# Kernel optimization log

Measured on AMD Instinct MI355X. Metric: run time of the kernel, lower is better.

The kernel has to match this reference:

```python
import jax, jax.numpy as jnp
import numpy as np

B, T, D = 2, 2048, 2048
H, HD = 8, 128
C = H * HD  # 1024 channels
BT = 64     # chunk size
EPS_RMS = 1.1920929e-07  # torch fp32 finfo eps (RMSNorm default)


def causal_dw_conv(x, w, b):
    # x: [B,T,C], w: [C,4], b: [C]. Equals torch Conv1d(groups=C, k=4, padding=3)[..., :T]
    Bx, Tx, Cx = x.shape
    xp = jnp.pad(x, ((0, 0), (3, 0), (0, 0)))
    out = sum(xp[:, j:j + Tx, :] * w[None, None, :, j] for j in range(4))
    return out + b


def chunk_kda(q, k, v, g):
    # q,k,g: [B,H,T,K]; v: [B,H,T,V]
    Bx, Hx, Tx, K = q.shape
    V = v.shape[-1]
    NT = Tx // BT
    resh = lambda a: a.reshape(Bx, Hx, NT, BT, a.shape[-1])
    q, k, v, g = map(resh, (q, k, v, g))
    gc = jnp.cumsum(g, axis=-2)                        # [B,H,NT,BT,K]
    diff = gc[..., :, None, :] - gc[..., None, :, :]   # [B,H,NT,BT,BT,K]
    tri_incl = jnp.tril(jnp.ones((BT, BT), bool))
    tri_strict = jnp.tril(jnp.ones((BT, BT), bool), -1)
    Aqk = jnp.einsum('bhnik,bhnjk,bhnijk->bhnij', q, k, jnp.exp(diff)) * tri_incl
    Akk = jnp.einsum('bhnik,bhnjk,bhnijk->bhnij', k, k, jnp.exp(-diff)) * tri_strict
    # UT transform: the in-place forward substitution in the source computes
    # A = (I + strictly_lower(Akk))^{-1}; apply it via a unit-lower triangular solve.
    M = Akk + jnp.eye(BT, dtype=q.dtype)
    rhs = jnp.concatenate([jnp.exp(gc) * k, v], axis=-1)
    sol = jax.scipy.linalg.solve_triangular(M, rhs, lower=True, unit_diagonal=True)
    w_, u = sol[..., :K], sol[..., K:]                 # w = A@(exp(gc)*k), u = A@v
    qg = q * jnp.exp(gc)

    def step(S, xs):
        qg_i, k_i, u_i, gc_i, w_i, Aqk_i = xs
        o_i = qg_i @ S + Aqk_i @ (u_i - w_i @ S)
        g_last = gc_i[:, :, -1]                        # [B,H,K]
        decay = jnp.exp(g_last[:, :, None, :] - gc_i)  # [B,H,BT,K]
        S = S * jnp.exp(g_last)[..., :, None] + jnp.einsum('bhck,bhcv->bhkv', k_i * decay, u_i)
        return S, o_i

    xs = tuple(jnp.moveaxis(a, 2, 0) for a in (qg, k, u, gc, w_, Aqk))
    S0 = jnp.zeros((Bx, Hx, K, V), q.dtype)
    S, o = jax.lax.scan(step, S0, xs)
    o = jnp.moveaxis(o, 0, 2).reshape(Bx, Hx, Tx, V)
    return o, S


def _forward(x, Wq, Wk, Wv, conv_q_w, conv_q_b, conv_k_w, conv_k_b, conv_v_w, conv_v_b,
             Wad, Wau, Wb, Wgd, Wgu, norm_w, Wo):
    Bx, Tx, Dx = x.shape
    heads = lambda y: y.reshape(Bx, Tx, H, HD).transpose(0, 2, 1, 3)
    q = heads(causal_dw_conv(x @ Wq, conv_q_w, conv_q_b))
    k = heads(causal_dw_conv(x @ Wk, conv_k_w, conv_k_b))
    q = q / jnp.maximum(jnp.linalg.norm(q, axis=-1, keepdims=True), 1e-12)
    k = k / jnp.maximum(jnp.linalg.norm(k, axis=-1, keepdims=True), 1e-12)
    v = heads(jax.nn.silu(causal_dw_conv(x @ Wv, conv_v_w, conv_v_b)))
    alpha = jax.nn.sigmoid(heads(x @ Wad @ Wau))
    g = jnp.log(jnp.clip(alpha, 1e-6, None))
    _beta = jax.nn.sigmoid(x @ Wb)  # computed in source but unused by chunk_kda
    o, S = chunk_kda(q, k, v, g)
    o = o.transpose(0, 2, 1, 3)                        # [B,T,H,HD]
    o = o * jax.lax.rsqrt(jnp.mean(o * o, axis=-1, keepdims=True) + EPS_RMS) * norm_w
    gate = jax.nn.sigmoid(x @ Wgd @ Wgu).reshape(Bx, Tx, H, HD)
    o = (o * gate).reshape(Bx, Tx, H * HD)
    return o @ Wo, S


def setup_inputs():
    key = jax.random.key(0)
    ks = jax.random.split(key, 16)
    n = lambda k, shape, s=0.02: jax.random.normal(k, shape, jnp.float32) * s
    return {
        'x': jax.random.normal(ks[0], (B, T, D), jnp.float32),
        'Wq': n(ks[1], (D, C)), 'Wk': n(ks[2], (D, C)), 'Wv': n(ks[3], (D, C)),
        'conv_q_w': n(ks[4], (C, 4), 0.1), 'conv_q_b': jnp.zeros((C,), jnp.float32),
        'conv_k_w': n(ks[5], (C, 4), 0.1), 'conv_k_b': jnp.zeros((C,), jnp.float32),
        'conv_v_w': n(ks[6], (C, 4), 0.1), 'conv_v_b': jnp.zeros((C,), jnp.float32),
        'Wad': n(ks[7], (D, HD)), 'Wau': n(ks[8], (HD, C)),
        'Wb': n(ks[9], (D, H)),
        'Wgd': n(ks[10], (D, HD)), 'Wgu': n(ks[11], (HD, C)),
        'norm_w': jnp.ones((HD,), jnp.float32),
        'Wo': n(ks[12], (C, D)),
    }


def reference(x, Wq, Wk, Wv, conv_q_w, conv_q_b, conv_k_w, conv_k_b, conv_v_w, conv_v_b,
              Wad, Wau, Wb, Wgd, Wgu, norm_w, Wo):
    return _forward(x, Wq, Wk, Wv, conv_q_w, conv_q_b, conv_k_w, conv_k_b, conv_v_w, conv_v_b,
                    Wad, Wau, Wb, Wgd, Wgu, norm_w, Wo)
```

## Files before the change

kernel.cpp:

```cpp
#include <hip/hip_runtime.h>
#include <hip/hip_bf16.h>
#include <cstdint>
#include <cstddef>

constexpr int B_  = 2;
constexpr int T_  = 2048;
constexpr int D_  = 2048;
constexpr int H_  = 8;
constexpr int HD_ = 128;
constexpr int C_  = 1024;
constexpr int BT_ = 64;
constexpr int NT_ = 32;
constexpr int M_  = 4096;
constexpr float EPS_RMS = 1.1920929e-07f;

typedef __bf16 bf16x8 __attribute__((ext_vector_type(8)));
typedef float f32x4 __attribute__((ext_vector_type(4)));

typedef const __attribute__((address_space(1))) unsigned int* gptr_t;
typedef __attribute__((address_space(3))) unsigned int* lptr_t;

__device__ __forceinline__ void gload16(const void* g, void* l) {
  __builtin_amdgcn_global_load_lds((gptr_t)g, (lptr_t)l, 16, 0, 0);
}


#define LD_A(base, mq, dst) do { \
    _Pragma("unroll") for (int i_ = 0; i_ < 4; ++i_) \
      _Pragma("unroll") for (int k_ = 0; k_ < 2; ++k_) \
        dst[i_][k_] = *(const bf16x8*)((base) + (mq) * 8192 + i_ * 2048 + k_ * 1024); \
  } while (0)

#define LD_B(base, nq, dst) do { \
    _Pragma("unroll") for (int j_ = 0; j_ < 2; ++j_) \
      _Pragma("unroll") for (int k_ = 0; k_ < 2; ++k_) \
        dst[j_][k_] = *(const bf16x8*)((base) + (nq) * 4096 + j_ * 2048 + k_ * 1024); \
  } while (0)

#define MM_Q(afr, bfr, mq, nq) do { \
    _Pragma("unroll") for (int i_ = 0; i_ < 4; ++i_) \
      _Pragma("unroll") for (int j_ = 0; j_ < 2; ++j_) \
        _Pragma("unroll") for (int k_ = 0; k_ < 2; ++k_) \
          acc[(mq) * 4 + i_][(nq) * 2 + j_] = __builtin_amdgcn_mfma_f32_16x16x32_bf16( \
              afr[i_][k_], bfr[j_][k_], acc[(mq) * 4 + i_][(nq) * 2 + j_], 0, 0, 0); \
  } while (0)

#define STAGE(src, grow0, kc, loff) do { \
    gload16((src) + (size_t)((grow0) + sr0) * 2048 + (kc) + sc0, smem + (loff) + tid * 16); \
    gload16((src) + (size_t)((grow0) + sr1) * 2048 + (kc) + sc1, smem + (loff) + 8192 + tid * 16); \
  } while (0)

#define PH_SYNC_PRE do { \
    __builtin_amdgcn_s_barrier(); \
    asm volatile("s_waitcnt lgkmcnt(0)" ::: "memory"); \
    __builtin_amdgcn_sched_barrier(0); \
    __builtin_amdgcn_s_setprio(1); \
  } while (0)

#define PH_SYNC_POST do { \
    __builtin_amdgcn_s_setprio(0); \
    __builtin_amdgcn_sched_barrier(0); \
    __builtin_amdgcn_s_barrier(); \
  } while (0)

#define PH_SYNC_POST_VM4 do { \
    __builtin_amdgcn_s_setprio(0); \
    __builtin_amdgcn_sched_barrier(0); \
    asm volatile("s_waitcnt vmcnt(4)" ::: "memory"); \
    __builtin_amdgcn_s_barrier(); \
  } while (0)

#define PH_SYNC_POST_VM0 do { \
    __builtin_amdgcn_s_setprio(0); \
    __builtin_amdgcn_sched_barrier(0); \
    asm volatile("s_waitcnt vmcnt(0)" ::: "memory"); \
    __builtin_amdgcn_s_barrier(); \
  } while (0)

__global__ __launch_bounds__(512, 1) void gemm8p(
    const __hip_bfloat16* __restrict__ A_, const __hip_bfloat16* __restrict__ B_,
    __hip_bfloat16* __restrict__ pre, __hip_bfloat16* __restrict__ adb,
    __hip_bfloat16* __restrict__ gdb) {
  __shared__ alignas(16) char smem[131072];
  const int tid = threadIdx.x, lane = tid & 63;
  const int wid = tid >> 6;
  const int wm = (wid >> 2) * 128, wn = (wid & 3) * 64;
  const int lr = lane & 15, lg = lane >> 4;

  const int bid = blockIdx.x;
  const int swz = (bid & 7) * 26 + (bid >> 3);
  const int mt = swz / 13, nt = swz % 13;
  const int m0 = mt * 256, n0g = nt * 256;

  int ob0 = tid * 16;         ob0 ^= ((ob0 >> 9) & 1) << 5;
  int ob1 = (tid + 512) * 16; ob1 ^= ((ob1 >> 9) & 1) << 5;
  const int sr0 = ((ob0 >> 11) << 4) + ((ob0 >> 6) & 15);
  const int sc0 = ((ob0 >> 10) & 1) * 32 + ((ob0 & 63) >> 1);
  const int sr1 = ((ob1 >> 11) << 4) + ((ob1 >> 6) & 15);
  const int sc1 = ((ob1 >> 10) & 1) * 32 + ((ob1 & 63) >> 1);

  const int foff = lr * 64 + ((lg * 16) ^ ((lr & 8) << 2));
  const int bq = (wn & 64) * 128;
  const char* a0base = smem + (wm >> 7) * 16384 + foff;
  const char* a1base = smem + 65536 + (wm >> 7) * 16384 + foff;
  const char* b0base = smem + 32768 + (wn >> 7) * 16384 + bq + foff;
  const char* b1base = smem + 98304 + (wn >> 7) * 16384 + bq + foff;

  f32x4 acc[8][4];
#pragma unroll
  for (int i = 0; i < 8; ++i)
#pragma unroll
    for (int j = 0; j < 4; ++j) acc[i][j] = (f32x4)(0.f);

  bf16x8 a[4][2], b01[2][2], b23[2][2];

  STAGE(A_, m0,        0, 0);
  STAGE(A_, m0 + 128,  0, 16384);
  STAGE(B_, n0g,       0, 32768);
  STAGE(B_, n0g + 128, 0, 32768 + 16384);
  STAGE(B_, n0g,       64, 98304);
  STAGE(B_, n0g + 128, 64, 98304 + 16384);
  asm volatile("s_waitcnt vmcnt(4)" ::: "memory");
  __builtin_amdgcn_s_barrier();

#pragma unroll 1
  for (int it = 0; it < 15; ++it) {
    const int kA1 = (2 * it + 1) * 64;
    const int kN2 = (2 * it + 2) * 64;
    const int kB3 = (2 * it + 3) * 64;
    LD_A(a0base, 0, a);
    LD_B(b0base, 0, b01);
    STAGE(A_, m0, kA1, 65536);
    PH_SYNC_PRE; MM_Q(a, b01, 0, 0); PH_SYNC_POST;
    LD_B(b0base, 1, b23);
    STAGE(A_, m0 + 128, kA1, 65536 + 16384);
    PH_SYNC_PRE; MM_Q(a, b23, 0, 1); PH_SYNC_POST;
    LD_A(a0base, 1, a);
    STAGE(B_, n0g, kN2, 32768);
    PH_SYNC_PRE; MM_Q(a, b23, 1, 1); PH_SYNC_POST;
    STAGE(B_, n0g + 128, kN2, 32768 + 16384);
    PH_SYNC_PRE; MM_Q(a, b01, 1, 0); PH_SYNC_POST_VM4;
    LD_A(a1base, 0, a);
    LD_B(b1base, 0, b01);
    STAGE(A_, m0, kN2, 0);
    PH_SYNC_PRE; MM_Q(a, b01, 0, 0); PH_SYNC_POST;
    LD_B(b1base, 1, b23);
    STAGE(A_, m0 + 128, kN2, 16384);
    PH_SYNC_PRE; MM_Q(a, b23, 0, 1); PH_SYNC_POST;
    LD_A(a1base, 1, a);
    STAGE(B_, n0g, kB3, 98304);
    PH_SYNC_PRE; MM_Q(a, b23, 1, 1); PH_SYNC_POST;
    STAGE(B_, n0g + 128, kB3, 98304 + 16384);
    PH_SYNC_PRE; MM_Q(a, b01, 1, 0); PH_SYNC_POST_VM4;
  }

  {
    const int kT = 1984;
    LD_A(a0base, 0, a);
    LD_B(b0base, 0, b01);
    STAGE(A_, m0, kT, 65536);
    PH_SYNC_PRE; MM_Q(a, b01, 0, 0); PH_SYNC_POST;
    LD_B(b0base, 1, b23);
    STAGE(A_, m0 + 128, kT, 65536 + 16384);
    PH_SYNC_PRE; MM_Q(a, b23, 0, 1); PH_SYNC_POST;
    LD_A(a0base, 1, a);
    PH_SYNC_PRE; MM_Q(a, b23, 1, 1); PH_SYNC_POST;
    PH_SYNC_PRE; MM_Q(a, b01, 1, 0); PH_SYNC_POST_VM0;
    LD_A(a1base, 0, a);
    LD_B(b1base, 0, b01);
    MM_Q(a, b01, 0, 0);
    LD_B(b1base, 1, b23);
    MM_Q(a, b23, 0, 1);
    LD_A(a1base, 1, a);
    MM_Q(a, b23, 1, 1);
    MM_Q(a, b01, 1, 0);
  }

#pragma unroll
  for (int mf = 0; mf < 8; ++mf) {
    const int row0 = m0 + wm + mf * 16 + lg * 4;
#pragma unroll
    for (int nf = 0; nf < 4; ++nf) {
      const int c = n0g + wn + nf * 16 + lr;
#pragma unroll
      for (int r = 0; r < 4; ++r) {
        const __hip_bfloat16 v = __float2bfloat16(acc[mf][nf][r]);
        const size_t rr = (size_t)(row0 + r);
        if (c < 3072)      pre[rr * 3072 + c] = v;
        else if (c < 3200) adb[rr * 128 + (c - 3072)] = v;
        else               gdb[rr * 128 + (c - 3200)] = v;
      }
    }
  }
}

template <typename OutT>
__global__ __launch_bounds__(256) void gemm_bf16k(
    const __hip_bfloat16* __restrict__ A, const __hip_bfloat16* __restrict__ Bt,
    OutT* __restrict__ C, int N, int K) {
  __shared__ __hip_bfloat16 sA[128 * 32];
  __shared__ __hip_bfloat16 sB[128 * 32];
  const int tid = threadIdx.x;
  const int lane = tid & 63;
  const int m0 = blockIdx.y * 128, n0 = blockIdx.x * 128;
  const int wm = ((tid >> 6) >> 1) * 64, wn = ((tid >> 6) & 1) * 64;
  f32x4 acc[4][4];
#pragma unroll
  for (int i = 0; i < 4; ++i)
#pragma unroll
    for (int j = 0; j < 4; ++j) acc[i][j] = (f32x4)(0.f);
  const int f0 = tid, f1 = tid + 256;
  const int r0 = f0 >> 2, c0 = (f0 & 3) * 8;
  const int r1 = f1 >> 2, c1 = (f1 & 3) * 8;
  const size_t aoff0 = (size_t)(m0 + r0) * K + c0;
  const size_t aoff1 = (size_t)(m0 + r1) * K + c1;
  const size_t boff0 = (size_t)(n0 + r0) * K + c0;
  const size_t boff1 = (size_t)(n0 + r1) * K + c1;
  const int lr = lane & 15, lk = (lane >> 4) * 8;
  for (int k0 = 0; k0 < K; k0 += 32) {
    __syncthreads();
    gload16(A + aoff0 + k0, &sA[f0 * 8]);
    gload16(A + aoff1 + k0, &sA[f1 * 8]);
    gload16(Bt + boff0 + k0, &sB[f0 * 8]);
    gload16(Bt + boff1 + k0, &sB[f1 * 8]);
    __syncthreads();
    bf16x8 af[4], bfr[4];
#pragma unroll
    for (int i = 0; i < 4; ++i)
      af[i] = *(const bf16x8*)&sA[(wm + i * 16 + lr) * 32 + lk];
#pragma unroll
    for (int j = 0; j < 4; ++j)
      bfr[j] = *(const bf16x8*)&sB[(wn + j * 16 + lr) * 32 + lk];
#pragma unroll
    for (int i = 0; i < 4; ++i)
#pragma unroll
      for (int j = 0; j < 4; ++j)
        acc[i][j] = __builtin_amdgcn_mfma_f32_16x16x32_bf16(af[i], bfr[j], acc[i][j], 0, 0, 0);
  }
  const int er = (lane >> 4) * 4, ec = lane & 15;
#pragma unroll
  for (int i = 0; i < 4; ++i) {
#pragma unroll
    for (int j = 0; j < 4; ++j) {
      int row = m0 + wm + i * 16 + er;
      int col = n0 + wn + j * 16 + ec;
#pragma unroll
      for (int r = 0; r < 4; ++r) {
        float v = acc[i][j][r];
        if constexpr (sizeof(OutT) == 2)
          C[(size_t)(row + r) * N + col] = __float2bfloat16(v);
        else
          C[(size_t)(row + r) * N + col] = v;
      }
    }
  }
}

__global__ __launch_bounds__(256) void gemm_augu(
    const __hip_bfloat16* __restrict__ ad, const __hip_bfloat16* __restrict__ gd,
    const __hip_bfloat16* __restrict__ Wau, const __hip_bfloat16* __restrict__ Wgu,
    float* __restrict__ a_full, __hip_bfloat16* __restrict__ gatef) {
  constexpr int N = 1024, K = 128;
  const int z = blockIdx.z;
  const __hip_bfloat16* A = z ? gd : ad;
  const __hip_bfloat16* Bt = z ? Wgu : Wau;
  __shared__ __hip_bfloat16 sA[128 * 32];
  __shared__ __hip_bfloat16 sB[128 * 32];
  const int tid = threadIdx.x;
  const int lane = tid & 63;
  const int m0 = blockIdx.y * 128, n0 = blockIdx.x * 128;
  const int wm = ((tid >> 6) >> 1) * 64, wn = ((tid >> 6) & 1) * 64;
  f32x4 acc[4][4];
#pragma unroll
  for (int i = 0; i < 4; ++i)
#pragma unroll
    for (int j = 0; j < 4; ++j) acc[i][j] = (f32x4)(0.f);
  const int f0 = tid, f1 = tid + 256;
  const int r0 = f0 >> 2, c0 = (f0 & 3) * 8;
  const int r1 = f1 >> 2, c1 = (f1 & 3) * 8;
  const size_t aoff0 = (size_t)(m0 + r0) * K + c0;
  const size_t aoff1 = (size_t)(m0 + r1) * K + c1;
  const size_t boff0 = (size_t)(n0 + r0) * K + c0;
  const size_t boff1 = (size_t)(n0 + r1) * K + c1;
  const int lr = lane & 15, lk = (lane >> 4) * 8;
#pragma unroll
  for (int k0 = 0; k0 < K; k0 += 32) {
    __syncthreads();
    gload16(A + aoff0 + k0, &sA[f0 * 8]);
    gload16(A + aoff1 + k0, &sA[f1 * 8]);
    gload16(Bt + boff0 + k0, &sB[f0 * 8]);
    gload16(Bt + boff1 + k0, &sB[f1 * 8]);
    __syncthreads();
    bf16x8 af[4], bfr[4];
#pragma unroll
    for (int i = 0; i < 4; ++i)
      af[i] = *(const bf16x8*)&sA[(wm + i * 16 + lr) * 32 + lk];
#pragma unroll
    for (int j = 0; j < 4; ++j)
      bfr[j] = *(const bf16x8*)&sB[(wn + j * 16 + lr) * 32 + lk];
#pragma unroll
    for (int i = 0; i < 4; ++i)
#pragma unroll
      for (int j = 0; j < 4; ++j)
        acc[i][j] = __builtin_amdgcn_mfma_f32_16x16x32_bf16(af[i], bfr[j], acc[i][j], 0, 0, 0);
  }
  const int er = (lane >> 4) * 4, ec = lane & 15;
#pragma unroll
  for (int i = 0; i < 4; ++i)
#pragma unroll
    for (int j = 0; j < 4; ++j) {
      int row = m0 + wm + i * 16 + er;
      int col = n0 + wn + j * 16 + ec;
#pragma unroll
      for (int r = 0; r < 4; ++r) {
        float v = acc[i][j][r];
        if (z == 0) a_full[(size_t)(row + r) * N + col] = v;
        else        gatef[(size_t)(row + r) * N + col] = __float2bfloat16(v);
      }
    }
}

__global__ __launch_bounds__(256) void prep(
    const float* __restrict__ x, const float* __restrict__ Wq,
    const float* __restrict__ Wk, const float* __restrict__ Wv,
    const float* __restrict__ Wad, const float* __restrict__ Wgd,
    const float* __restrict__ Wau, const float* __restrict__ Wgu,
    const float* __restrict__ Wo, __hip_bfloat16* __restrict__ xb,
    __hip_bfloat16* __restrict__ Wt_qkv, __hip_bfloat16* __restrict__ Wt_dg,
    __hip_bfloat16* __restrict__ Wt_aug, __hip_bfloat16* __restrict__ Wt_o) {
  __shared__ float tile[32][33];
  int bid = blockIdx.x;
  const int tid = threadIdx.x;
  if (bid < 8192) {
    size_t i = ((size_t)bid * 256 + tid) * 4;
    float4 v = *(const float4*)(x + i);
    xb[i + 0] = __float2bfloat16(v.x);
    xb[i + 1] = __float2bfloat16(v.y);
    xb[i + 2] = __float2bfloat16(v.z);
    xb[i + 3] = __float2bfloat16(v.w);
    return;
  }
  bid -= 8192;
  const float* W; __hip_bfloat16* dst; int K, N, bx, by;
  if (bid < 6144) {
    int z = bid / 2048, r = bid % 2048;
    W = (z == 0) ? Wq : (z == 1) ? Wk : Wv;
    dst = Wt_qkv + (size_t)z * C_ * D_;
    K = D_; N = C_; bx = r & 31; by = r >> 5;
  } else if (bid < 6144 + 512) {
    int b2 = bid - 6144;
    int z = b2 >> 8, r = b2 & 255;
    W = z ? Wgd : Wad;
    dst = Wt_dg + (size_t)z * HD_ * D_;
    K = D_; N = HD_; bx = r & 3; by = r >> 2;
  } else if (bid < 6144 + 512 + 256) {
    int b2 = bid - 6144 - 512;
    int z = b2 >> 7, r = b2 & 127;
    W = z ? Wgu : Wau;
    dst = Wt_aug + (size_t)z * C_ * HD_;
    K = HD_; N = C_; bx = r & 31; by = r >> 5;
  } else {
    int b2 = bid - 6144 - 512 - 256;
    W = Wo; dst = Wt_o;
    K = C_; N = D_; bx = b2 & 63; by = b2 >> 6;
  }
  int tx = tid & 31, ty = tid >> 5;
  int kb = by * 32, nb = bx * 32;
#pragma unroll
  for (int s = 0; s < 4; ++s) {
    int kk = ty + s * 8;
    tile[kk][tx] = W[(size_t)(kb + kk) * N + nb + tx];
  }
  __syncthreads();
#pragma unroll
  for (int s = 0; s < 4; ++s) {
    int nn = ty + s * 8;
    dst[(size_t)(nb + nn) * K + kb + tx] = __float2bfloat16(tile[tx][nn]);
  }
}

__global__ __launch_bounds__(256) void gc_lds(
    const float* __restrict__ a_full, float* __restrict__ gc,
    float* __restrict__ glast) {
  __shared__ float gcS[64][128];
  const int tid = threadIdx.x;
  const int bhn = blockIdx.x;
  const int bh = bhn >> 5, n = bhn & 31;
  const int b = bh >> 3, h = bh & 7;
  const int t0 = n * 64, hoff = h * 128;
  for (int ci = tid; ci < 2048; ci += 256) {
    int r = ci >> 5, c4 = (ci & 31) * 4;
    *(float4*)&gcS[r][c4] =
        *(const float4*)(a_full + (size_t)(b * T_ + t0 + r) * C_ + hoff + c4);
  }
  __syncthreads();
  if (tid < 128) {
    float run = 0.f;
    for (int i = 0; i < 64; ++i) {
      float a = gcS[i][tid];
      float s = fmaxf(1.f / (1.f + __expf(-a)), 1e-6f);
      run += __logf(s);
      gcS[i][tid] = run;
    }
    glast[(size_t)bhn * 128 + tid] = run;
  }
  __syncthreads();
  const size_t gbase = ((size_t)bh * T_ + t0) * 128;
  for (int ci = tid; ci < 2048; ci += 256) {
    int r = ci >> 5, c4 = (ci & 31) * 4;
    *(float4*)(gc + gbase + r * 128 + c4) = *(const float4*)&gcS[r][c4];
  }
}

__global__ __launch_bounds__(128) void conv_qkv(
    const __hip_bfloat16* __restrict__ pre, const float* __restrict__ gc,
    const float* __restrict__ cqw, const float* __restrict__ cqb,
    const float* __restrict__ ckw, const float* __restrict__ ckb,
    const float* __restrict__ cvw, const float* __restrict__ cvb,
    __hip_bfloat16* __restrict__ qg, __hip_bfloat16* __restrict__ kp,
    __hip_bfloat16* __restrict__ km, __hip_bfloat16* __restrict__ vb) {
  int idx = blockIdx.x;
  int h = idx & 7;
  int t = (idx >> 3) & (T_ - 1);
  int b = idx >> 14;
  int d = threadIdx.x;
  int c = h * HD_ + d;
  const __hip_bfloat16* p = pre + (size_t)(b * T_ + t) * (3 * C_) + c;
  float aq, ak, av;
  {
    float w0 = cqw[c * 4], w1 = cqw[c * 4 + 1], w2 = cqw[c * 4 + 2], w3 = cqw[c * 4 + 3];
    aq = cqb[c] + w3 * __bfloat162float(p[0]);
    if (t > 0) aq += w2 * __bfloat162float(p[-(ptrdiff_t)(3 * C_)]);
    if (t > 1) aq += w1 * __bfloat162float(p[-2 * (ptrdiff_t)(3 * C_)]);
    if (t > 2) aq += w0 * __bfloat162float(p[-3 * (ptrdiff_t)(3 * C_)]);
  }
  {
    const __hip_bfloat16* pk = p + C_;
    float w0 = ckw[c * 4], w1 = ckw[c * 4 + 1], w2 = ckw[c * 4 + 2], w3 = ckw[c * 4 + 3];
    ak = ckb[c] + w3 * __bfloat162float(pk[0]);
    if (t > 0) ak += w2 * __bfloat162float(pk[-(ptrdiff_t)(3 * C_)]);
    if (t > 1) ak += w1 * __bfloat162float(pk[-2 * (ptrdiff_t)(3 * C_)]);
    if (t > 2) ak += w0 * __bfloat162float(pk[-3 * (ptrdiff_t)(3 * C_)]);
  }
  {
    const __hip_bfloat16* pv = p + 2 * C_;
    float w0 = cvw[c * 4], w1 = cvw[c * 4 + 1], w2 = cvw[c * 4 + 2], w3 = cvw[c * 4 + 3];
    av = cvb[c] + w3 * __bfloat162float(pv[0]);
    if (t > 0) av += w2 * __bfloat162float(pv[-(ptrdiff_t)(3 * C_)]);
    if (t > 1) av += w1 * __bfloat162float(pv[-2 * (ptrdiff_t)(3 * C_)]);
    if (t > 2) av += w0 * __bfloat162float(pv[-3 * (ptrdiff_t)(3 * C_)]);
  }
  float ssq = aq * aq, ssk = ak * ak;
#pragma unroll
  for (int o = 1; o < 64; o <<= 1) {
    ssq += __shfl_xor(ssq, o);
    ssk += __shfl_xor(ssk, o);
  }
  __shared__ float red[2][2];
  if ((d & 63) == 0) { red[0][d >> 6] = ssq; red[1][d >> 6] = ssk; }
  __syncthreads();
  float nq = fmaxf(sqrtf(red[0][0] + red[0][1]), 1e-12f);
  float nk = fmaxf(sqrtf(red[1][0] + red[1][1]), 1e-12f);
  size_t oi = (((size_t)b * H_ + h) * T_ + t) * HD_ + d;
  float g = gc[oi];
  float eg = __expf(g), emg = __expf(-g);
  qg[oi] = __float2bfloat16(aq / nq * eg);
  float kn = ak / nk;
  kp[oi] = __float2bfloat16(kn * eg);
  km[oi] = __float2bfloat16(kn * emg);
  vb[oi] = __float2bfloat16(av * (1.f / (1.f + __expf(-av))));
}

__global__ __launch_bounds__(256) void chunk_mid(
    const __hip_bfloat16* __restrict__ qg, const __hip_bfloat16* __restrict__ kp,
    const __hip_bfloat16* __restrict__ km, const __hip_bfloat16* __restrict__ vb,
    __hip_bfloat16* __restrict__ Aq, __hip_bfloat16* __restrict__ w_bf,
    __hip_bfloat16* __restrict__ u_bf, __hip_bfloat16* __restrict__ PT_bf) {
  __shared__ float A_T[64][68];
  __shared__ float solu[64][128];
  const int tid = threadIdx.x;
  const int bhn = blockIdx.x;
  const size_t gbase = ((size_t)(bhn >> 5) * T_ + (size_t)(bhn & 31) * BT_) * HD_;
  const int wv = tid >> 6, lane = tid & 63;
  const int lr = lane & 15, lg = lane >> 4;
  const int prod = wv >> 1, rh = wv & 1;

  {
    const __hip_bfloat16* A = (prod ? qg : km) + gbase;
    const __hip_bfloat16* Bt = (prod ? km : kp) + gbase;
    f32x4 acc[2][4];
#pragma unroll
    for (int i = 0; i < 2; ++i)
#pragma unroll
      for (int j = 0; j < 4; ++j) acc[i][j] = (f32x4)(0.f);
#pragma unroll
    for (int k0 = 0; k0 < 128; k0 += 32) {
      bf16x8 af[2], bfr[4];
#pragma unroll
      for (int i = 0; i < 2; ++i)
        af[i] = *(const bf16x8*)(A + (size_t)(rh * 32 + i * 16 + lr) * 128 + k0 + lg * 8);
#pragma unroll
      for (int j = 0; j < 4; ++j)
        bfr[j] = *(const bf16x8*)(Bt + (size_t)(j * 16 + lr) * 128 + k0 + lg * 8);
#pragma unroll
      for (int i = 0; i < 2; ++i)
#pragma unroll
        for (int j = 0; j < 4; ++j)
          acc[i][j] = __builtin_amdgcn_mfma_f32_16x16x32_bf16(af[i], bfr[j], acc[i][j], 0, 0, 0);
    }
    if (prod == 0) {
#pragma unroll
      for (int i = 0; i < 2; ++i)
#pragma unroll
        for (int j = 0; j < 4; ++j) {
          int row0 = rh * 32 + i * 16 + lg * 4;
          int col = j * 16 + lr;
          *(float4*)&A_T[col][row0] =
              make_float4(acc[i][j][0], acc[i][j][1], acc[i][j][2], acc[i][j][3]);
        }
    } else {
      __hip_bfloat16* dst = Aq + (size_t)bhn * 4096;
#pragma unroll
      for (int i = 0; i < 2; ++i)
#pragma unroll
        for (int j = 0; j < 4; ++j)
#pragma unroll
          for (int r = 0; r < 4; ++r) {
            int row = rh * 32 + i * 16 + lg * 4 + r;
            int col = j * 16 + lr;
            float v = (col <= row) ? acc[i][j][r] : 0.f;
            dst[row * 64 + col] = __float2bfloat16(v);
          }
    }
  }
  __syncthreads();

  {
    const int col = tid & 127;
    const __hip_bfloat16* rhs = ((tid < 128) ? kp : vb) + gbase;
    float s[64];
#pragma unroll
    for (int i = 0; i < 64; ++i)
      s[i] = __bfloat162float(rhs[(size_t)i * 128 + col]);
#pragma unroll
    for (int ib = 0; ib < 64; ib += 4) {
      const float s0 = s[ib];
      const float s1 = fmaf(-A_T[ib][ib + 1], s0, s[ib + 1]);
      const float s2 = fmaf(-A_T[ib + 1][ib + 2], s1,
                       fmaf(-A_T[ib][ib + 2], s0, s[ib + 2]));
      const float s3 = fmaf(-A_T[ib + 2][ib + 3], s2,
                       fmaf(-A_T[ib + 1][ib + 3], s1,
                       fmaf(-A_T[ib][ib + 3], s0, s[ib + 3])));
      s[ib + 1] = s1; s[ib + 2] = s2; s[ib + 3] = s3;
#pragma unroll
      for (int j4 = ib + 4; j4 < 64; j4 += 4) {
        float4 a0 = *(const float4*)&A_T[ib][j4];
        float4 a1 = *(const float4*)&A_T[ib + 1][j4];
        float4 a2 = *(const float4*)&A_T[ib + 2][j4];
        float4 a3 = *(const float4*)&A_T[ib + 3][j4];
        s[j4]     = fmaf(-a3.x, s3, fmaf(-a2.x, s2, fmaf(-a1.x, s1, fmaf(-a0.x, s0, s[j4]))));
        s[j4 + 1] = fmaf(-a3.y, s3, fmaf(-a2.y, s2, fmaf(-a1.y, s1, fmaf(-a0.y, s0, s[j4 + 1]))));
        s[j4 + 2] = fmaf(-a3.z, s3, fmaf(-a2.z, s2, fmaf(-a1.z, s1, fmaf(-a0.z, s0, s[j4 + 2]))));
        s[j4 + 3] = fmaf(-a3.w, s3, fmaf(-a2.w, s2, fmaf(-a1.w, s1, fmaf(-a0.w, s0, s[j4 + 3]))));
      }
    }
    if (tid < 128) {
#pragma unroll
      for (int i = 0; i < 64; ++i)
        w_bf[gbase + (size_t)i * 128 + col] = __float2bfloat16(s[i]);
    } else {
#pragma unroll
      for (int i = 0; i < 64; ++i) {
        u_bf[gbase + (size_t)i * 128 + col] = __float2bfloat16(s[i]);
        solu[i][col] = s[i];
      }
    }
  }
  __syncthreads();

  {
    const int kd0 = (tid & 15) * 8, vd0 = (tid >> 4) * 8;
    float acc[8][8];
#pragma unroll
    for (int a = 0; a < 8; ++a)
#pragma unroll
      for (int b2 = 0; b2 < 8; ++b2) acc[a][b2] = 0.f;
    for (int i = 0; i < 64; ++i) {
      uint4 rawv = *(const uint4*)(km + gbase + (size_t)i * 128 + kd0);
      const __hip_bfloat16* hp = (const __hip_bfloat16*)&rawv;
      float kv[8];
#pragma unroll
      for (int e = 0; e < 8; ++e) kv[e] = __bfloat162float(hp[e]);
      float uv[8];
      *(float4*)(uv)     = *(const float4*)&solu[i][vd0];
      *(float4*)(uv + 4) = *(const float4*)&solu[i][vd0 + 4];
#pragma unroll
      for (int a = 0; a < 8; ++a)
#pragma unroll
        for (int b2 = 0; b2 < 8; ++b2) acc[a][b2] = fmaf(kv[a], uv[b2], acc[a][b2]);
    }
    __hip_bfloat16* dst = PT_bf + (size_t)bhn * 16384;
#pragma unroll
    for (int b2 = 0; b2 < 8; ++b2) {
      union { __hip_bfloat16 hx[8]; uint4 u4; } pk2;
#pragma unroll
      for (int a = 0; a < 8; ++a) pk2.hx[a] = __float2bfloat16(acc[a][b2]);
      *(uint4*)(dst + (size_t)(vd0 + b2) * 128 + kd0) = pk2.u4;
    }
  }
}

__global__ __launch_bounds__(128) void scan_pt(
    const __hip_bfloat16* __restrict__ PT_bf, const float* __restrict__ glast,
    __hip_bfloat16* __restrict__ STg, float* __restrict__ Sout) {
  int vd = blockIdx.x & 127;
  int bh = blockIdx.x >> 7;
  int kd = threadIdx.x;
  float s = 0.f;
  for (int n = 0; n < NT_; ++n) {
    size_t idx = (((size_t)bh * NT_ + n) * HD_ + vd) * HD_ + kd;
    float p = __bfloat162float(PT_bf[idx]);
    STg[idx] = __float2bfloat16(s);
    float gl = glast[((size_t)bh * NT_ + n) * 128 + kd];
    s = (s + p) * __expf(gl);
  }
  Sout[((size_t)bh * HD_ + kd) * HD_ + vd] = s;
}

__global__ __launch_bounds__(256) void chunk_tail(
    const __hip_bfloat16* __restrict__ qg_bf, const __hip_bfloat16* __restrict__ w_bf,
    const __hip_bfloat16* __restrict__ u_bf, const __hip_bfloat16* __restrict__ Aq_bf,
    const __hip_bfloat16* __restrict__ STg, const __hip_bfloat16* __restrict__ gatef,
    const float* __restrict__ normw, __hip_bfloat16* __restrict__ o2b) {
  constexpr int XTS = 72;
  __shared__ __hip_bfloat16 XT[128 * XTS];
  __shared__ float red[64][4];
  const int tid = threadIdx.x;
  const int bhn = blockIdx.x;
  const int bh = bhn >> 5, n = bhn & 31;
  const int b = bh >> 3, h = bh & 7;
  const int t0 = n * 64, hoff = h * 128;
  const size_t gbase = ((size_t)bh * T_ + t0) * 128;
  const __hip_bfloat16* Sg = STg + (size_t)bhn * 16384;

  const int wv = tid >> 6, lane = tid & 63;
  const int lr = lane & 15, lg = lane >> 4;
  f32x4 accX[4][2], accO[4][2];
#pragma unroll
  for (int i = 0; i < 4; ++i)
#pragma unroll
    for (int j = 0; j < 2; ++j) { accX[i][j] = (f32x4)(0.f); accO[i][j] = (f32x4)(0.f); }

  const __hip_bfloat16* wrow = w_bf + gbase;
  const __hip_bfloat16* qrow = qg_bf + gbase;
#pragma unroll
  for (int k0 = 0; k0 < 128; k0 += 32) {
    bf16x8 aW[4], aQ[4], bS[2];
#pragma unroll
    for (int i = 0; i < 4; ++i) {
      aW[i] = *(const bf16x8*)(wrow + (size_t)(i * 16 + lr) * 128 + k0 + lg * 8);
      aQ[i] = *(const bf16x8*)(qrow + (size_t)(i * 16 + lr) * 128 + k0 + lg * 8);
    }
#pragma unroll
    for (int j = 0; j < 2; ++j)
      bS[j] = *(const bf16x8*)(Sg + (size_t)(wv * 32 + j * 16 + lr) * 128 + k0 + lg * 8);
#pragma unroll
    for (int i = 0; i < 4; ++i)
#pragma unroll
      for (int j = 0; j < 2; ++j) {
        accX[i][j] = __builtin_amdgcn_mfma_f32_16x16x32_bf16(aW[i], bS[j], accX[i][j], 0, 0, 0);
        accO[i][j] = __builtin_amdgcn_mfma_f32_16x16x32_bf16(aQ[i], bS[j], accO[i][j], 0, 0, 0);
      }
  }

#pragma unroll
  for (int i = 0; i < 4; ++i)
#pragma unroll
    for (int j = 0; j < 2; ++j) {
      int row0 = i * 16 + lg * 4;
      int col = wv * 32 + j * 16 + lr;
      union { __hip_bfloat16 hx[4]; uint2 u2; } xv;
#pragma unroll
      for (int r = 0; r < 4; ++r) {
        float uu = __bfloat162float(u_bf[gbase + (size_t)(row0 + r) * 128 + col]);
        xv.hx[r] = __float2bfloat16(uu - accX[i][j][r]);
      }
      *(uint2*)&XT[col * XTS + row0] = xv.u2;
    }
  __syncthreads();

  const __hip_bfloat16* aqb = Aq_bf + (size_t)bhn * 4096;
#pragma unroll
  for (int k0 = 0; k0 < 64; k0 += 32) {
    bf16x8 aA[4], bX[2];
#pragma unroll
    for (int i = 0; i < 4; ++i)
      aA[i] = *(const bf16x8*)(aqb + (size_t)(i * 16 + lr) * 64 + k0 + lg * 8);
#pragma unroll
    for (int j = 0; j < 2; ++j)
      bX[j] = *(const bf16x8*)&XT[(wv * 32 + j * 16 + lr) * XTS + k0 + lg * 8];
#pragma unroll
    for (int i = 0; i < 4; ++i)
#pragma unroll
      for (int j = 0; j < 2; ++j)
        accO[i][j] = __builtin_amdgcn_mfma_f32_16x16x32_bf16(aA[i], bX[j], accO[i][j], 0, 0, 0);
  }

#pragma unroll
  for (int i = 0; i < 4; ++i)
#pragma unroll
    for (int r = 0; r < 4; ++r) {
      int row = i * 16 + lg * 4 + r;
      float o0 = accO[i][0][r], o1 = accO[i][1][r];
      float ss = o0 * o0 + o1 * o1;
#pragma unroll
      for (int o = 1; o < 16; o <<= 1) ss += __shfl_xor(ss, o);
      if (lr == 0) red[row][wv] = ss;
    }
  __syncthreads();
  float nw0 = normw[wv * 32 + lr];
  float nw1 = normw[wv * 32 + 16 + lr];
#pragma unroll
  for (int i = 0; i < 4; ++i)
#pragma unroll
    for (int r = 0; r < 4; ++r) {
      int row = i * 16 + lg * 4 + r;
      float tot = red[row][0] + red[row][1] + red[row][2] + red[row][3];
      float rms = rsqrtf(tot * (1.f / 128.f) + EPS_RMS);
      size_t orow = (size_t)(b * T_ + t0 + row) * C_ + hoff;
      int c0 = wv * 32 + lr, c1 = c0 + 16;
      float g0 = __bfloat162float(gatef[orow + c0]);
      float g1 = __bfloat162float(gatef[orow + c1]);
      float s0 = 1.f / (1.f + __expf(-g0));
      float s1 = 1.f / (1.f + __expf(-g1));
      o2b[orow + c0] = __float2bfloat16(accO[i][0][r] * rms * nw0 * s0);
      o2b[orow + c1] = __float2bfloat16(accO[i][1][r] * rms * nw1 * s1);
    }
}

extern "C" void kernel_launch(void* const* d_in, const int* in_sizes, int n_in,
                              void* d_out, int out_size, void* d_ws, size_t ws_size,
                              hipStream_t stream) {
  (void)in_sizes; (void)n_in; (void)out_size;
  const float* x    = (const float*)d_in[0];
  const float* Wq   = (const float*)d_in[1];
  const float* Wk   = (const float*)d_in[2];
  const float* Wv   = (const float*)d_in[3];
  const float* cqw  = (const float*)d_in[4];
  const float* cqb  = (const float*)d_in[5];
  const float* ckw  = (const float*)d_in[6];
  const float* ckb  = (const float*)d_in[7];
  const float* cvw  = (const float*)d_in[8];
  const float* cvb  = (const float*)d_in[9];
  const float* Wad  = (const float*)d_in[10];
  const float* Wau  = (const float*)d_in[11];
  const float* Wgd  = (const float*)d_in[13];
  const float* Wgu  = (const float*)d_in[14];
  const float* normw= (const float*)d_in[15];
  const float* Wo   = (const float*)d_in[16];

  float* outp = (float*)d_out;
  float* Sout = outp + (size_t)M_ * D_;

  const size_t SZ = (size_t)M_ * C_;

  float* ws = (float*)d_ws;
  __hip_bfloat16* pre_qkv = (__hip_bfloat16*)(ws);
  float* a_full = ws + 3 * SZ / 2;
  __hip_bfloat16* gatef = (__hip_bfloat16*)(ws + 5 * SZ / 2);
  float* gc_g = ws + 3 * SZ;
  __hip_bfloat16* qg_bf = (__hip_bfloat16*)(ws + 4 * SZ);
  __hip_bfloat16* kp_bf = (__hip_bfloat16*)(ws + 9 * SZ / 2);
  __hip_bfloat16* km_bf = (__hip_bfloat16*)(ws + 5 * SZ);
  __hip_bfloat16* v_bf  = (__hip_bfloat16*)(ws + 11 * SZ / 2);
  __hip_bfloat16* w_bf  = (__hip_bfloat16*)(ws + 6 * SZ);
  __hip_bfloat16* u_bf  = (__hip_bfloat16*)(ws + 13 * SZ / 2);
  __hip_bfloat16* Aq_bf = (__hip_bfloat16*)(ws + 7 * SZ);
  float* glast = ws + 29 * SZ / 4;
  __hip_bfloat16* PT_bf = (__hip_bfloat16*)(ws + 15 * SZ / 2);
  __hip_bfloat16* STg   = (__hip_bfloat16*)(ws + 17 * SZ / 2);
  __hip_bfloat16* xb    = (__hip_bfloat16*)(ws + 19 * SZ / 2);
  __hip_bfloat16* Wt_qkv = (__hip_bfloat16*)(ws + 21 * SZ / 2);
  size_t off = 21 * SZ / 2 + 3 * SZ / 4;
  __hip_bfloat16* Wt_dg  = (__hip_bfloat16*)(ws + off); off += 262144;
  __hip_bfloat16* Wt_aug = (__hip_bfloat16*)(ws + off); off += 131072;
  __hip_bfloat16* Wt_o   = (__hip_bfloat16*)(ws + off); off += 1048576;
  __hip_bfloat16* ad_bf  = (__hip_bfloat16*)(ws + off); off += 262144;
  __hip_bfloat16* gd_bf  = (__hip_bfloat16*)(ws + off); off += 262144;
  if (ws_size < off * sizeof(float)) return;

  __hip_bfloat16* o2b = (__hip_bfloat16*)a_full;
  __hip_bfloat16* Wt_au = Wt_aug;
  __hip_bfloat16* Wt_gu = Wt_aug + (size_t)C_ * HD_;

  prep<<<17152, 256, 0, stream>>>(x, Wq, Wk, Wv, Wad, Wgd, Wau, Wgu, Wo,
                                  xb, Wt_qkv, Wt_dg, Wt_aug, Wt_o);

  gemm8p<<<208, 512, 0, stream>>>(xb, Wt_qkv, pre_qkv, ad_bf, gd_bf);
  gemm_augu<<<dim3(C_ / 128, M_ / 128, 2), 256, 0, stream>>>(
      ad_bf, gd_bf, Wt_au, Wt_gu, a_full, gatef);

  gc_lds<<<B_ * H_ * NT_, 256, 0, stream>>>(a_full, gc_g, glast);
  conv_qkv<<<B_ * T_ * H_, 128, 0, stream>>>(pre_qkv, gc_g, cqw, cqb, ckw, ckb,
                                             cvw, cvb, qg_bf, kp_bf, km_bf, v_bf);

  chunk_mid<<<B_ * H_ * NT_, 256, 0, stream>>>(qg_bf, kp_bf, km_bf, v_bf,
                                               Aq_bf, w_bf, u_bf, PT_bf);
  scan_pt<<<B_ * H_ * HD_, 128, 0, stream>>>(PT_bf, glast, STg, Sout);

  chunk_tail<<<B_ * H_ * NT_, 256, 0, stream>>>(qg_bf, w_bf, u_bf, Aq_bf, STg,
                                                gatef, normw, o2b);
  gemm_bf16k<float><<<dim3(D_ / 128, M_ / 128), 256, 0, stream>>>(o2b, Wt_o, outp, D_, C_);
}
```

Before: 372.9 us.

## Fuse gate log-sigmoid cumsum into augu GEMM epilogue and stage km/u in LDS

Drops the separate gc_lds kernel. The gemm_augu epilogue for the a-branch now computes log-sigmoid into shared memory, then does the per-chunk cumulative sum and writes gc and glast directly, so the fp32 a_full round trip and one launch go away. It also prefetches km in chunk_mid and u in chunk_tail into LDS with async global-to-LDS loads, replacing scattered global reads. The cost is more LDS per block and a serial 64-step scan carried by all 256 threads in the GEMM epilogue.

```diff
diff --git a/kernel.cpp b/kernel.cpp
--- a/kernel.cpp
+++ b/kernel.cpp
@@ -259,13 +259,17 @@
 __global__ __launch_bounds__(256) void gemm_augu(
     const __hip_bfloat16* __restrict__ ad, const __hip_bfloat16* __restrict__ gd,
     const __hip_bfloat16* __restrict__ Wau, const __hip_bfloat16* __restrict__ Wgu,
-    float* __restrict__ a_full, __hip_bfloat16* __restrict__ gatef) {
+    float* __restrict__ gc, float* __restrict__ glast,
+    __hip_bfloat16* __restrict__ gatef) {
   constexpr int N = 1024, K = 128;
+  __shared__ alignas(16) char smraw[128 * 132 * 4];
+  __hip_bfloat16* sA = (__hip_bfloat16*)smraw;
+  __hip_bfloat16* sB = (__hip_bfloat16*)(smraw + 8192);
+  float (*scan)[132] = (float(*)[132])smraw;
+
   const int z = blockIdx.z;
   const __hip_bfloat16* A = z ? gd : ad;
   const __hip_bfloat16* Bt = z ? Wgu : Wau;
-  __shared__ __hip_bfloat16 sA[128 * 32];
-  __shared__ __hip_bfloat16 sB[128 * 32];
   const int tid = threadIdx.x;
   const int lane = tid & 63;
   const int m0 = blockIdx.y * 128, n0 = blockIdx.x * 128;
@@ -305,19 +309,47 @@
         acc[i][j] = __builtin_amdgcn_mfma_f32_16x16x32_bf16(af[i], bfr[j], acc[i][j], 0, 0, 0);
   }
   const int er = (lane >> 4) * 4, ec = lane & 15;
+  if (z == 1) {
+#pragma unroll
+    for (int i = 0; i < 4; ++i)
+#pragma unroll
+      for (int j = 0; j < 4; ++j) {
+        int row = m0 + wm + i * 16 + er;
+        int col = n0 + wn + j * 16 + ec;
+#pragma unroll
+        for (int r = 0; r < 4; ++r)
+          gatef[(size_t)(row + r) * N + col] = __float2bfloat16(acc[i][j][r]);
+      }
+    return;
+  }
+  __syncthreads();
 #pragma unroll
   for (int i = 0; i < 4; ++i)
 #pragma unroll
     for (int j = 0; j < 4; ++j) {
-      int row = m0 + wm + i * 16 + er;
-      int col = n0 + wn + j * 16 + ec;
+      int rowL = wm + i * 16 + er;
+      int colL = wn + j * 16 + ec;
 #pragma unroll
       for (int r = 0; r < 4; ++r) {
-        float v = acc[i][j][r];
-        if (z == 0) a_full[(size_t)(row + r) * N + col] = v;
-        else        gatef[(size_t)(row + r) * N + col] = __float2bfloat16(v);
+        float a = acc[i][j][r];
+        float s = fmaxf(1.f / (1.f + __expf(-a)), 1e-6f);
+        scan[rowL + r][colL] = __logf(s);
       }
     }
+  __syncthreads();
+  {
+    const int d = tid & 127, c2 = tid >> 7;
+    const int h = blockIdx.x;
+    const int b = m0 >> 11, tb = m0 & 2047;
+    const int bh = b * H_ + h;
+    float run = 0.f;
+    const size_t gbase = ((size_t)bh * T_ + tb + c2 * 64) * 128 + d;
+    for (int r = 0; r < 64; ++r) {
+      run += scan[c2 * 64 + r][d];
+      gc[gbase + (size_t)r * 128] = run;
+    }
+    glast[((size_t)(bh * NT_ + (tb >> 6) + c2)) * 128 + d] = run;
+  }
 }
 
 __global__ __launch_bounds__(256) void prep(
@@ -379,39 +411,6 @@
   }
 }
 
-__global__ __launch_bounds__(256) void gc_lds(
-    const float* __restrict__ a_full, float* __restrict__ gc,
-    float* __restrict__ glast) {
-  __shared__ float gcS[64][128];
-  const int tid = threadIdx.x;
-  const int bhn = blockIdx.x;
-  const int bh = bhn >> 5, n = bhn & 31;
-  const int b = bh >> 3, h = bh & 7;
-  const int t0 = n * 64, hoff = h * 128;
-  for (int ci = tid; ci < 2048; ci += 256) {
-    int r = ci >> 5, c4 = (ci & 31) * 4;
-    *(float4*)&gcS[r][c4] =
-        *(const float4*)(a_full + (size_t)(b * T_ + t0 + r) * C_ + hoff + c4);
-  }
-  __syncthreads();
-  if (tid < 128) {
-    float run = 0.f;
-    for (int i = 0; i < 64; ++i) {
-      float a = gcS[i][tid];
-      float s = fmaxf(1.f / (1.f + __expf(-a)), 1e-6f);
-      run += __logf(s);
-      gcS[i][tid] = run;
-    }
-    glast[(size_t)bhn * 128 + tid] = run;
-  }
-  __syncthreads();
-  const size_t gbase = ((size_t)bh * T_ + t0) * 128;
-  for (int ci = tid; ci < 2048; ci += 256) {
-    int r = ci >> 5, c4 = (ci & 31) * 4;
-    *(float4*)(gc + gbase + r * 128 + c4) = *(const float4*)&gcS[r][c4];
-  }
-}
-
 __global__ __launch_bounds__(128) void conv_qkv(
     const __hip_bfloat16* __restrict__ pre, const float* __restrict__ gc,
     const float* __restrict__ cqw, const float* __restrict__ cqb,
@@ -478,12 +477,20 @@
     __hip_bfloat16* __restrict__ u_bf, __hip_bfloat16* __restrict__ PT_bf) {
   __shared__ float A_T[64][68];
   __shared__ float solu[64][128];
+  __shared__ __hip_bfloat16 kmS[64 * 128];
   const int tid = threadIdx.x;
   const int bhn = blockIdx.x;
   const size_t gbase = ((size_t)(bhn >> 5) * T_ + (size_t)(bhn & 31) * BT_) * HD_;
   const int wv = tid >> 6, lane = tid & 63;
   const int lr = lane & 15, lg = lane >> 4;
   const int prod = wv >> 1, rh = wv & 1;
+
+  {
+    const char* src = (const char*)(km + gbase);
+#pragma unroll
+    for (int s = 0; s < 4; ++s)
+      gload16(src + s * 4096 + tid * 16, ((char*)kmS) + s * 4096 + tid * 16);
+  }
 
   {
     const __hip_bfloat16* A = (prod ? qg : km) + gbase;
@@ -585,8 +592,9 @@
     for (int a = 0; a < 8; ++a)
 #pragma unroll
       for (int b2 = 0; b2 < 8; ++b2) acc[a][b2] = 0.f;
+#pragma unroll 4
     for (int i = 0; i < 64; ++i) {
-      uint4 rawv = *(const uint4*)(km + gbase + (size_t)i * 128 + kd0);
+      uint4 rawv = *(const uint4*)&kmS[i * 128 + kd0];
       const __hip_bfloat16* hp = (const __hip_bfloat16*)&rawv;
       float kv[8];
 #pragma unroll
@@ -635,6 +643,7 @@
   constexpr int XTS = 72;
   __shared__ __hip_bfloat16 XT[128 * XTS];
   __shared__ float red[64][4];
+  __shared__ __hip_bfloat16 uS[64 * 128];
   const int tid = threadIdx.x;
   const int bhn = blockIdx.x;
   const int bh = bhn >> 5, n = bhn & 31;
@@ -643,6 +652,13 @@
   const size_t gbase = ((size_t)bh * T_ + t0) * 128;
   const __hip_bfloat16* Sg = STg + (size_t)bhn * 16384;
 
+  {
+    const char* src = (const char*)(u_bf + gbase);
+#pragma unroll
+    for (int s = 0; s < 4; ++s)
+      gload16(src + s * 4096 + tid * 16, ((char*)uS) + s * 4096 + tid * 16);
+  }
+
   const int wv = tid >> 6, lane = tid & 63;
   const int lr = lane & 15, lg = lane >> 4;
   f32x4 accX[4][2], accO[4][2];
@@ -673,6 +689,9 @@
       }
   }
 
+  asm volatile("s_waitcnt vmcnt(0)" ::: "memory");
+  __builtin_amdgcn_s_barrier();
+
 #pragma unroll
   for (int i = 0; i < 4; ++i)
 #pragma unroll
@@ -682,7 +701,7 @@
       union { __hip_bfloat16 hx[4]; uint2 u2; } xv;
 #pragma unroll
       for (int r = 0; r < 4; ++r) {
-        float uu = __bfloat162float(u_bf[gbase + (size_t)(row0 + r) * 128 + col]);
+        float uu = __bfloat162float(uS[(row0 + r) * 128 + col]);
         xv.hx[r] = __float2bfloat16(uu - accX[i][j][r]);
       }
       *(uint2*)&XT[col * XTS + row0] = xv.u2;
@@ -798,9 +817,8 @@
 
   gemm8p<<<208, 512, 0, stream>>>(xb, Wt_qkv, pre_qkv, ad_bf, gd_bf);
   gemm_augu<<<dim3(C_ / 128, M_ / 128, 2), 256, 0, stream>>>(
-      ad_bf, gd_bf, Wt_au, Wt_gu, a_full, gatef);
-
-  gc_lds<<<B_ * H_ * NT_, 256, 0, stream>>>(a_full, gc_g, glast);
+      ad_bf, gd_bf, Wt_au, Wt_gu, gc_g, glast, gatef);
+
   conv_qkv<<<B_ * T_ * H_, 128, 0, stream>>>(pre_qkv, gc_g, cqw, cqb, ckw, ckb,
                                              cvw, cvb, qg_bf, kp_bf, km_bf, v_bf);
 
```

Result: faster. 362.2 us (-2.9%).
